# Kernel optimization log

Measured on AMD Instinct MI355X. Metric: run time of the kernel, lower is better.

The kernel has to match this reference:

```python
import jax, jax.numpy as jnp
import numpy as np

KH, KW = 3, 3
STRIDE = (1, 1)
PAD = (1, 1)
DIL = (1, 1)


def setup_inputs() -> dict:
    key = jax.random.key(0)
    k1, k2, k3, k4 = jax.random.split(key, 4)
    B, Cin, H, W = 8, 256, 64, 64
    Cout = 256
    x = jax.random.normal(k1, (B, Cin, H, W), jnp.float32)
    offset = jax.random.normal(k2, (B, 2 * KH * KW, H, W), jnp.float32)
    fan_in = Cin * KH * KW
    bound = 1.0 / np.sqrt(fan_in).astype(np.float32)
    weight = jax.random.uniform(k3, (Cout, Cin, KH, KW), jnp.float32, -bound, bound)
    bias = jax.random.uniform(k4, (Cout,), jnp.float32, -bound, bound)
    return {"x": x, "offset": offset, "weight": weight, "bias": bias}


def _deform_conv2d(x, offset, weight, bias):
    B, Cin, H, W = x.shape
    Cout = weight.shape[0]
    Ho, Wo = offset.shape[2], offset.shape[3]
    # offset layout: [B, 2*KH*KW, Ho, Wo] -> (dy, dx) per kernel tap
    off = offset.reshape(B, KH, KW, 2, Ho, Wo)
    dy = off[:, :, :, 0]  # [B,KH,KW,Ho,Wo]
    dx = off[:, :, :, 1]
    grid_y = jnp.arange(Ho, dtype=x.dtype) * STRIDE[0] - PAD[0]  # [Ho]
    grid_x = jnp.arange(Wo, dtype=x.dtype) * STRIDE[1] - PAD[1]  # [Wo]
    ker_y = jnp.arange(KH, dtype=x.dtype) * DIL[0]  # [KH]
    ker_x = jnp.arange(KW, dtype=x.dtype) * DIL[1]  # [KW]
    # sampling positions [B,KH,KW,Ho,Wo]
    py = dy + grid_y[None, None, None, :, None] + ker_y[None, :, None, None, None]
    px = dx + grid_x[None, None, None, None, :] + ker_x[None, None, :, None, None]

    y0f = jnp.floor(py)
    x0f = jnp.floor(px)
    wy = py - y0f  # fractional weights
    wx = px - x0f
    y0 = y0f.astype(jnp.int32)
    x0 = x0f.astype(jnp.int32)

    x_flat = x.reshape(B, Cin, H * W)

    def corner(yi, xi, w):
        # bilinear corner with zero padding outside the image
        valid = (yi >= 0) & (yi < H) & (xi >= 0) & (xi < W)
        idx = jnp.clip(yi, 0, H - 1) * W + jnp.clip(xi, 0, W - 1)  # [B,KH,KW,Ho,Wo]
        vals = jax.vmap(lambda xf, ii: xf[:, ii])(x_flat, idx)  # [B,Cin,KH,KW,Ho,Wo]
        return vals * (w * valid)[:, None]

    acc = corner(y0, x0, (1 - wy) * (1 - wx))
    acc = acc + corner(y0, x0 + 1, (1 - wy) * wx)
    acc = acc + corner(y0 + 1, x0, wy * (1 - wx))
    acc = acc + corner(y0 + 1, x0 + 1, wy * wx)

    # convolution accumulation over (Cin, KH, KW)
    out = jnp.einsum('bckluv,ockl->bouv', acc, weight)
    return out + bias[None, :, None, None]


def reference(x, offset, weight, bias):
    return _deform_conv2d(x, offset, weight, bias)
```

## Files before the change

kernel.cpp:

```cpp
#include <hip/hip_runtime.h>
#include <hip/hip_bf16.h>
#include <stdint.h>

typedef __attribute__((ext_vector_type(8))) short s16x8;
typedef __attribute__((ext_vector_type(4))) float f32x4;

#define XT_OFF   0u
#define WT_OFF   16777216u
#define PW_OFF   17956864u
#define PI_OFF   22675456u
#define WS_NEED  25034752u

static __device__ __forceinline__ uint16_t f2bf(float f) {
    __hip_bfloat16 h = __float2bfloat16(f);
    uint16_t u;
    __builtin_memcpy(&u, &h, 2);
    return u;
}
static __device__ __forceinline__ float bflo(uint32_t w) { return __uint_as_float(w << 16); }
static __device__ __forceinline__ float bfhi(uint32_t w) { return __uint_as_float(w & 0xffff0000u); }
static __device__ __forceinline__ float rdl(float v, int l) {
    return __uint_as_float((uint32_t)__builtin_amdgcn_readlane((int)__float_as_uint(v), l));
}

__global__ __launch_bounds__(256) void k_transpose_x(const float* __restrict__ x,
                                                     uint16_t* __restrict__ xt) {
    __shared__ float tile[64][65];
    const int blk = blockIdx.x;
    const int b   = blk >> 8;
    const int yxt = (blk >> 2) & 63;
    const int ct  = blk & 3;
    const int yx0 = yxt << 6, c0 = ct << 6;
    const int tx  = threadIdx.x;
    const int ty  = tx >> 6, lx = tx & 63;
    #pragma unroll
    for (int i = 0; i < 16; ++i) {
        const int c = (i << 2) + ty;
        tile[c][lx] = x[(size_t)((b * 256 + c0 + c) << 12) + yx0 + lx];
    }
    __syncthreads();
    const int cpr = lx & 31;
    #pragma unroll
    for (int i = 0; i < 8; ++i) {
        const int r = (ty << 1) + (lx >> 5) + (i << 3);
        const uint32_t lo = f2bf(tile[2 * cpr][r]);
        const uint32_t hi = f2bf(tile[2 * cpr + 1][r]);
        *(uint32_t*)&xt[(size_t)(b * 4096 + yx0 + r) * 256 + c0 + 2 * cpr] = lo | (hi << 16);
    }
}

__global__ __launch_bounds__(256) void k_prep_w(const float* __restrict__ wgt,
                                                uint16_t* __restrict__ wt) {
    const int blk = blockIdx.x;
    const int kb = blk >> 2, wc = blk & 3;
    const int m = threadIdx.x >> 6, lane = threadIdx.x & 63;
    const int o = wc * 64 + m * 16 + (lane & 15);
    const int t = kb >> 3;
    const int ch0 = (kb & 7) * 32 + (lane >> 4) * 8;
    uint32_t pk[4];
    #pragma unroll
    for (int q = 0; q < 4; ++q) {
        const float v0 = wgt[(size_t)o * 2304 + (size_t)(ch0 + 2 * q) * 9 + t];
        const float v1 = wgt[(size_t)o * 2304 + (size_t)(ch0 + 2 * q + 1) * 9 + t];
        pk[q] = (uint32_t)f2bf(v0) | ((uint32_t)f2bf(v1) << 16);
    }
    uint4 r; r.x = pk[0]; r.y = pk[1]; r.z = pk[2]; r.w = pk[3];
    *(uint4*)((char*)wt + (size_t)kb * 16384 + wc * 4096 + m * 1024 + lane * 16) = r;
}

__global__ __launch_bounds__(256) void k_prep_params(const float* __restrict__ off,
                                                     float4* __restrict__ pw,
                                                     uint2* __restrict__ pi) {
    const int blk = blockIdx.x;
    const int b = blk / 144;
    const int r = blk - b * 144;
    const int t = r >> 4;
    const int p = ((r & 15) << 8) + threadIdx.x;
    const int u = p >> 6, v = p & 63;
    const int kh = t / 3, kw = t - 3 * kh;
    const float dy = off[(size_t)((b * 18 + 2 * t) << 12) + p];
    const float dx = off[(size_t)((b * 18 + 2 * t + 1) << 12) + p];
    const float py = dy + (float)(u - 1 + kh);
    const float px = dx + (float)(v - 1 + kw);
    const float y0f = floorf(py), x0f = floorf(px);
    const float wy = py - y0f, wx = px - x0f;
    const int y0 = (int)y0f, x0 = (int)x0f;
    const int y1 = y0 + 1, x1 = x0 + 1;
    const bool vy0 = (y0 >= 0) && (y0 < 64);
    const bool vy1 = (y1 >= 0) && (y1 < 64);
    const bool vx0 = (x0 >= 0) && (x0 < 64);
    const bool vx1 = (x1 >= 0) && (x1 < 64);
    const int cy0 = min(max(y0, 0), 63), cy1 = min(max(y1, 0), 63);
    const int cx0 = min(max(x0, 0), 63), cx1 = min(max(x1, 0), 63);
    float4 w4;
    w4.x = (1.f - wy) * (1.f - wx) * ((vy0 && vx0) ? 1.f : 0.f);
    w4.y = (1.f - wy) * wx         * ((vy0 && vx1) ? 1.f : 0.f);
    w4.z = wy * (1.f - wx)         * ((vy1 && vx0) ? 1.f : 0.f);
    w4.w = wy * wx                 * ((vy1 && vx1) ? 1.f : 0.f);
    uint2 id;
    id.x = (uint32_t)(cy0 * 64 + cx0) | ((uint32_t)(cy0 * 64 + cx1) << 16);
    id.y = (uint32_t)(cy1 * 64 + cx0) | ((uint32_t)(cy1 * 64 + cx1) << 16);
    const size_t o_ = (size_t)(b * 9 + t) * 4096 + p;
    pw[o_] = w4;
    pi[o_] = id;
}


#define BLENDPX(PAR, LP, PXL) do {                                                \
    const float wqa = rdl(pwv.x, (PXL)), wqb = rdl(pwv.y, (PXL));                 \
    const float wqc = rdl(pwv.z, (PXL)), wqd = rdl(pwv.w, (PXL));                 \
    const uint2 A_ = cr[PAR][0], B_ = cr[PAR][1];                                 \
    const uint2 C_ = cr[PAR][2], D_ = cr[PAR][3];                                 \
    uint2 r_;                                                                     \
    { const float lo = wqa * bflo(A_.x) + wqb * bflo(B_.x)                        \
                     + wqc * bflo(C_.x) + wqd * bflo(D_.x);                       \
      const float hi = wqa * bfhi(A_.x) + wqb * bfhi(B_.x)                        \
                     + wqc * bfhi(C_.x) + wqd * bfhi(D_.x);                       \
      r_.x = (uint32_t)f2bf(lo) | ((uint32_t)f2bf(hi) << 16); }                   \
    { const float lo = wqa * bflo(A_.y) + wqb * bflo(B_.y)                        \
                     + wqc * bflo(C_.y) + wqd * bflo(D_.y);                       \
      const float hi = wqa * bfhi(A_.y) + wqb * bfhi(B_.y)                        \
                     + wqc * bfhi(C_.y) + wqd * bfhi(D_.y);                       \
      r_.y = (uint32_t)f2bf(lo) | ((uint32_t)f2bf(hi) << 16); }                   \
    const int slot_ = (lane >> 1) ^ ((LP) & 7);                                   \
    *(uint2*)(inxt + (LP) * 512 + slot_ * 16 + (lane & 1) * 8) = r_;              \
} while (0)

#define STEP(T, S, STG) do {                                                      \
    const int kb_ = (T) * 8 + (S);                                                \
    if (STG) {                                                                    \
        const uint32_t ix_ = (uint32_t)__builtin_amdgcn_readlane((int)piv.x, (S)); \
        const uint32_t iy_ = (uint32_t)__builtin_amdgcn_readlane((int)piv.y, (S)); \
        cr[(S)&1][0] = *(const uint2*)(xb + (ix_ & 0xffffu) * 256u + lane * 4);   \
        cr[(S)&1][1] = *(const uint2*)(xb + (ix_ >> 16)     * 256u + lane * 4);   \
        cr[(S)&1][2] = *(const uint2*)(xb + (iy_ & 0xffffu) * 256u + lane * 4);   \
        cr[(S)&1][3] = *(const uint2*)(xb + (iy_ >> 16)     * 256u + lane * 4);   \
    }                                                                             \
    if (kb_ < 71) {                                                               \
        _Pragma("unroll")                                                         \
        for (int m = 0; m < 4; ++m)                                               \
            wA[((S)+1)&1][m] = *(const s16x8*)(wfrag + (size_t)(kb_+1) * 16384 + m * 1024); \
    }                                                                             \
    if ((STG) && (S) >= 1) BLENDPX(((S)-1)&1, wv * 8 + (S) - 1, (S) - 1);         \
    {                                                                             \
        s16x8 bfr[2];                                                             \
        _Pragma("unroll")                                                         \
        for (int j = 0; j < 2; ++j)                                               \
            bfr[j] = *(const s16x8*)(icur + rb0 + j * 8192 + ((((S) * 4 + kp) ^ (l15 & 7)) << 4)); \
        __builtin_amdgcn_s_setprio(1);                                            \
        _Pragma("unroll")                                                         \
        for (int m = 0; m < 4; ++m)                                               \
            _Pragma("unroll")                                                     \
            for (int j = 0; j < 2; ++j)                                           \
                acc[m][j] = __builtin_amdgcn_mfma_f32_16x16x32_bf16(wA[(S)&1][m], bfr[j], acc[m][j], 0, 0, 0); \
        __builtin_amdgcn_s_setprio(0);                                            \
    }                                                                             \
} while (0)

__global__ __launch_bounds__(512, 4) void k_main(const uint16_t* __restrict__ xt,
                                                 const uint16_t* __restrict__ wt,
                                                 const float4* __restrict__ pw,
                                                 const uint2* __restrict__ pi,
                                                 const float* __restrict__ bias,
                                                 float* __restrict__ out) {
    __shared__ uint16_t imc[2][64 * 256];

    const int orig = blockIdx.x;
    const int bid  = (orig & 7) * 64 + (orig >> 3);
    const int b    = bid >> 6;
    const int pix0 = (bid & 63) << 6;

    const int tx   = threadIdx.x;
    const int lane = tx & 63;
    const int wv   = tx >> 6;
    const int wc   = wv & 3;
    const int wn   = wv >> 2;
    const int l15  = lane & 15;
    const int kp   = lane >> 4;

    const uint16_t* xb = xt + (size_t)b * 4096 * 256;
    const char* wfrag = (const char*)wt + (size_t)wc * 4096 + (size_t)lane * 16;

    const int rb0 = (wn * 32 + l15) * 512;

    f32x4 acc[4][2];
    #pragma unroll
    for (int m = 0; m < 4; ++m)
        #pragma unroll
        for (int j = 0; j < 2; ++j) acc[m][j] = (f32x4){0.f, 0.f, 0.f, 0.f};

    #pragma unroll
    for (int i = 0; i < 8; ++i) {
        const int lp = wv * 8 + i;
        const int ui = __builtin_amdgcn_readfirstlane(b * 9 * 4096 + pix0 + lp);
        const uint2  id = pi[ui];
        const float4 w4 = pw[ui];
        const uint2 A  = *(const uint2*)(xb + (id.x & 0xffffu) * 256u + lane * 4);
        const uint2 Bv = *(const uint2*)(xb + (id.x >> 16)     * 256u + lane * 4);
        const uint2 Cv = *(const uint2*)(xb + (id.y & 0xffffu) * 256u + lane * 4);
        const uint2 Dv = *(const uint2*)(xb + (id.y >> 16)     * 256u + lane * 4);
        uint2 r;
        { const float lo = w4.x * bflo(A.x) + w4.y * bflo(Bv.x)
                         + w4.z * bflo(Cv.x) + w4.w * bflo(Dv.x);
          const float hi = w4.x * bfhi(A.x) + w4.y * bfhi(Bv.x)
                         + w4.z * bfhi(Cv.x) + w4.w * bfhi(Dv.x);
          r.x = (uint32_t)f2bf(lo) | ((uint32_t)f2bf(hi) << 16); }
        { const float lo = w4.x * bflo(A.y) + w4.y * bflo(Bv.y)
                         + w4.z * bflo(Cv.y) + w4.w * bflo(Dv.y);
          const float hi = w4.x * bfhi(A.y) + w4.y * bfhi(Bv.y)
                         + w4.z * bfhi(Cv.y) + w4.w * bfhi(Dv.y);
          r.y = (uint32_t)f2bf(lo) | ((uint32_t)f2bf(hi) << 16); }
        const int slot = (lane >> 1) ^ (lp & 7);
        *(uint2*)((char*)&imc[0][0] + lp * 512 + slot * 16 + (lane & 1) * 8) = r;
    }

    s16x8 wA[2][4];
    #pragma unroll
    for (int m = 0; m < 4; ++m) wA[0][m] = *(const s16x8*)(wfrag + m * 1024);

    uint2  cr[2][4];
    uint2  piv = {0, 0};
    float4 pwv = {0.f, 0.f, 0.f, 0.f};

    #pragma unroll 1
    for (int t = 0; t < 8; ++t) {
        __syncthreads();
        const char* icur = (const char*)&imc[t & 1][0];
        char*       inxt = (char*)&imc[(t + 1) & 1][0];
        {
            const int idx = (b * 9 + t + 1) * 4096 + pix0 + wv * 8 + (lane & 7);
            piv = pi[idx];
            pwv = pw[idx];
        }
        STEP(t, 0, 1); STEP(t, 1, 1); STEP(t, 2, 1); STEP(t, 3, 1);
        STEP(t, 4, 1); STEP(t, 5, 1); STEP(t, 6, 1); STEP(t, 7, 1);
        BLENDPX(1, wv * 8 + 7, 7);
    }

    __syncthreads();
    {
        const char* icur = (const char*)&imc[0][0];
        char*       inxt = (char*)&imc[1][0];
        (void)inxt;
        STEP(8, 0, 0); STEP(8, 1, 0); STEP(8, 2, 0); STEP(8, 3, 0);
        STEP(8, 4, 0); STEP(8, 5, 0); STEP(8, 6, 0); STEP(8, 7, 0);
    }

    #pragma unroll
    for (int m = 0; m < 4; ++m) {
        #pragma unroll
        for (int q = 0; q < 4; ++q) {
            const int o = wc * 64 + m * 16 + kp * 4 + q;
            const float bv = bias[o];
            float* orow = out + (((size_t)(b * 256 + o)) << 12) + pix0 + wn * 32;
            #pragma unroll
            for (int j = 0; j < 2; ++j)
                orow[j * 16 + l15] = acc[m][j][q] + bv;
        }
    }
}

#define KTOT 2304
#define KCF  32
#define WROW 260
#define AROW 72

__global__ __launch_bounds__(256) void deform_conv_fallback(
    const float* __restrict__ x, const float* __restrict__ off,
    const float* __restrict__ wgt, const float* __restrict__ bias,
    float* __restrict__ out) {
    __shared__ float  w_lds[KCF][WROW];
    __shared__ float  a_lds[KCF][AROW];
    __shared__ int4   pidx[9][64];
    __shared__ float4 pwgt[9][64];
    const int tx = threadIdx.x;
    const int blk = blockIdx.x;
    const int b = blk >> 6, u = blk & 63;
    for (int item = tx; item < 9 * 64; item += 256) {
        const int t = item >> 6, p = item & 63;
        const int k = t / 3, l = t - 3 * k;
        const float dy = off[((b * 18 + 2 * t) << 12) + u * 64 + p];
        const float dx = off[((b * 18 + 2 * t + 1) << 12) + u * 64 + p];
        const float py = dy + (float)(u - 1 + k);
        const float px = dx + (float)(p - 1 + l);
        const float y0f = floorf(py), x0f = floorf(px);
        const float wy = py - y0f, wx = px - x0f;
        const int y0 = (int)y0f, x0 = (int)x0f, y1 = y0 + 1, x1 = x0 + 1;
        const bool vy0 = (y0 >= 0) && (y0 < 64), vy1 = (y1 >= 0) && (y1 < 64);
        const bool vx0 = (x0 >= 0) && (x0 < 64), vx1 = (x1 >= 0) && (x1 < 64);
        const int cy0 = min(max(y0, 0), 63), cy1 = min(max(y1, 0), 63);
        const int cx0 = min(max(x0, 0), 63), cx1 = min(max(x1, 0), 63);
        int4 id; id.x = cy0 * 64 + cx0; id.y = cy0 * 64 + cx1;
        id.z = cy1 * 64 + cx0; id.w = cy1 * 64 + cx1;
        float4 w4;
        w4.x = (1.f - wy) * (1.f - wx) * ((vy0 && vx0) ? 1.f : 0.f);
        w4.y = (1.f - wy) * wx * ((vy0 && vx1) ? 1.f : 0.f);
        w4.z = wy * (1.f - wx) * ((vy1 && vx0) ? 1.f : 0.f);
        w4.w = wy * wx * ((vy1 && vx1) ? 1.f : 0.f);
        pidx[t][p] = id; pwgt[t][p] = w4;
    }
    const int og = tx & 31, pgr = tx >> 5;
    float acc[8][8];
    #pragma unroll
    for (int j = 0; j < 8; ++j)
        #pragma unroll
        for (int q = 0; q < 8; ++q) acc[j][q] = 0.f;
    __syncthreads();
    for (int kb = 0; kb < 72; ++kb) {
        const int k0 = kb * KCF;
        #pragma unroll
        for (int it = 0; it < 8; ++it) {
            const int item = it * 256 + tx;
            const int o = item >> 3, jj = item & 7;
            const float4 v = *(const float4*)&wgt[o * KTOT + k0 + jj * 4];
            w_lds[jj * 4 + 0][o] = v.x; w_lds[jj * 4 + 1][o] = v.y;
            w_lds[jj * 4 + 2][o] = v.z; w_lds[jj * 4 + 3][o] = v.w;
        }
        #pragma unroll
        for (int it = 0; it < 8; ++it) {
            const int item = it * 256 + tx;
            const int kk = item >> 6, p = item & 63;
            const int kg = k0 + kk;
            const int c = kg / 9, t = kg - 9 * c;
            const float* plane = x + ((b * 256 + c) << 12);
            const int4 id = pidx[t][p];
            const float4 w4 = pwgt[t][p];
            float v = w4.x * plane[id.x] + w4.y * plane[id.y]
                    + w4.z * plane[id.z] + w4.w * plane[id.w];
            a_lds[kk][p] = v;
        }
        __syncthreads();
        #pragma unroll 2
        for (int kk = 0; kk < KCF; ++kk) {
            const float4 w0 = *(const float4*)&w_lds[kk][og * 8];
            const float4 w1 = *(const float4*)&w_lds[kk][og * 8 + 4];
            const float4 a0 = *(const float4*)&a_lds[kk][pgr * 8];
            const float4 a1 = *(const float4*)&a_lds[kk][pgr * 8 + 4];
            const float wv[8] = {w0.x, w0.y, w0.z, w0.w, w1.x, w1.y, w1.z, w1.w};
            const float av[8] = {a0.x, a0.y, a0.z, a0.w, a1.x, a1.y, a1.z, a1.w};
            #pragma unroll
            for (int j = 0; j < 8; ++j)
                #pragma unroll
                for (int q = 0; q < 8; ++q) acc[j][q] += wv[j] * av[q];
        }
        __syncthreads();
    }
    const int vb = pgr * 8;
    #pragma unroll
    for (int j = 0; j < 8; ++j) {
        const int o = og * 8 + j;
        const float bv = bias[o];
        float* op = out + ((b * 256 + o) << 12) + u * 64 + vb;
        float4 r0, r1;
        r0.x = acc[j][0] + bv; r0.y = acc[j][1] + bv; r0.z = acc[j][2] + bv; r0.w = acc[j][3] + bv;
        r1.x = acc[j][4] + bv; r1.y = acc[j][5] + bv; r1.z = acc[j][6] + bv; r1.w = acc[j][7] + bv;
        *(float4*)op = r0; *(float4*)(op + 4) = r1;
    }
}

extern "C" void kernel_launch(void* const* d_in, const int* in_sizes, int n_in,
                              void* d_out, int out_size, void* d_ws, size_t ws_size,
                              hipStream_t stream) {
    const float* x    = (const float*)d_in[0];
    const float* off  = (const float*)d_in[1];
    const float* wgt  = (const float*)d_in[2];
    const float* bias = (const float*)d_in[3];
    float* out = (float*)d_out;

    if (ws_size < WS_NEED) {
        deform_conv_fallback<<<dim3(512), dim3(256), 0, stream>>>(x, off, wgt, bias, out);
        return;
    }
    uint16_t* xt  = (uint16_t*)((char*)d_ws + XT_OFF);
    uint16_t* wtp = (uint16_t*)((char*)d_ws + WT_OFF);
    float4*   pwp = (float4*)((char*)d_ws + PW_OFF);
    uint2*    pip = (uint2*)((char*)d_ws + PI_OFF);

    k_transpose_x <<<dim3(2048), dim3(256), 0, stream>>>(x, xt);
    k_prep_w      <<<dim3(288),  dim3(256), 0, stream>>>(wgt, wtp);
    k_prep_params <<<dim3(1152), dim3(256), 0, stream>>>(off, pwp, pip);
    k_main        <<<dim3(512),  dim3(512), 0, stream>>>(xt, wtp, pwp, pip, bias, out);
}
```

Before: 97.31 us.

## Re-tile waves to 32 out-channels x 64 pixels and pair k-steps per stage

Changes the per-wave MFMA tile from 64 output channels x 32 pixels to 32 output channels x 64 pixels, so each wave reads all pixel columns from LDS and a narrower weight slice. The weight prep layout is regrouped into 16-channel groups to match. The main loop now processes two k-blocks per step, gathering corners for two pixels at once and blending two pixels per step, which deepens the prefetch of gathered data and weights. This trades more LDS B-fragment reads per wave for fewer global weight loads, and holds more gathered registers at once, which may raise register pressure.

```diff
diff --git a/kernel.cpp b/kernel.cpp
--- a/kernel.cpp
+++ b/kernel.cpp
@@ -52,9 +52,10 @@
 __global__ __launch_bounds__(256) void k_prep_w(const float* __restrict__ wgt,
                                                 uint16_t* __restrict__ wt) {
     const int blk = blockIdx.x;
-    const int kb = blk >> 2, wc = blk & 3;
+    const int kb = blk >> 2, gq = blk & 3;
     const int m = threadIdx.x >> 6, lane = threadIdx.x & 63;
-    const int o = wc * 64 + m * 16 + (lane & 15);
+    const int g = gq * 4 + m;
+    const int o = g * 16 + (lane & 15);
     const int t = kb >> 3;
     const int ch0 = (kb & 7) * 32 + (lane >> 4) * 8;
     uint32_t pk[4];
@@ -65,7 +66,7 @@
         pk[q] = (uint32_t)f2bf(v0) | ((uint32_t)f2bf(v1) << 16);
     }
     uint4 r; r.x = pk[0]; r.y = pk[1]; r.z = pk[2]; r.w = pk[3];
-    *(uint4*)((char*)wt + (size_t)kb * 16384 + wc * 4096 + m * 1024 + lane * 16) = r;
+    *(uint4*)((char*)wt + (size_t)kb * 16384 + g * 1024 + lane * 16) = r;
 }
 
 __global__ __launch_bounds__(256) void k_prep_params(const float* __restrict__ off,
@@ -106,11 +107,13 @@
 }
 
 
-#define BLENDPX(PAR, LP, PXL) do {                                                \
+#define BOFF(S) ((((S) * 4 + kp) ^ (l15 & 7)) << 4)
+
+#define BLEND1(SLOT, P, PXL) do {                                                 \
     const float wqa = rdl(pwv.x, (PXL)), wqb = rdl(pwv.y, (PXL));                 \
     const float wqc = rdl(pwv.z, (PXL)), wqd = rdl(pwv.w, (PXL));                 \
-    const uint2 A_ = cr[PAR][0], B_ = cr[PAR][1];                                 \
-    const uint2 C_ = cr[PAR][2], D_ = cr[PAR][3];                                 \
+    const uint2 A_ = cr[SLOT][P][0], B_ = cr[SLOT][P][1];                         \
+    const uint2 C_ = cr[SLOT][P][2], D_ = cr[SLOT][P][3];                         \
     uint2 r_;                                                                     \
     { const float lo = wqa * bflo(A_.x) + wqb * bflo(B_.x)                        \
                      + wqc * bflo(C_.x) + wqd * bflo(D_.x);                       \
@@ -122,37 +125,58 @@
       const float hi = wqa * bfhi(A_.y) + wqb * bfhi(B_.y)                        \
                      + wqc * bfhi(C_.y) + wqd * bfhi(D_.y);                       \
       r_.y = (uint32_t)f2bf(lo) | ((uint32_t)f2bf(hi) << 16); }                   \
-    const int slot_ = (lane >> 1) ^ ((LP) & 7);                                   \
-    *(uint2*)(inxt + (LP) * 512 + slot_ * 16 + (lane & 1) * 8) = r_;              \
+    const int lp_ = wv * 8 + (PXL);                                               \
+    const int sl_ = (lane >> 1) ^ (lp_ & 7);                                      \
+    *(uint2*)(inxt + lp_ * 512 + sl_ * 16 + (lane & 1) * 8) = r_;                 \
 } while (0)
 
-#define STEP(T, S, STG) do {                                                      \
-    const int kb_ = (T) * 8 + (S);                                                \
-    if (STG) {                                                                    \
-        const uint32_t ix_ = (uint32_t)__builtin_amdgcn_readlane((int)piv.x, (S)); \
-        const uint32_t iy_ = (uint32_t)__builtin_amdgcn_readlane((int)piv.y, (S)); \
-        cr[(S)&1][0] = *(const uint2*)(xb + (ix_ & 0xffffu) * 256u + lane * 4);   \
-        cr[(S)&1][1] = *(const uint2*)(xb + (ix_ >> 16)     * 256u + lane * 4);   \
-        cr[(S)&1][2] = *(const uint2*)(xb + (iy_ & 0xffffu) * 256u + lane * 4);   \
-        cr[(S)&1][3] = *(const uint2*)(xb + (iy_ >> 16)     * 256u + lane * 4);   \
+#define ISSUE2(SLOT, PX0) do {                                                    \
+    _Pragma("unroll")                                                             \
+    for (int p_ = 0; p_ < 2; ++p_) {                                              \
+        const uint32_t ix_ = (uint32_t)__builtin_amdgcn_readlane((int)piv.x, (PX0) + p_); \
+        const uint32_t iy_ = (uint32_t)__builtin_amdgcn_readlane((int)piv.y, (PX0) + p_); \
+        cr[SLOT][p_][0] = *(const uint2*)(xb + (ix_ & 0xffffu) * 256u + lane * 4); \
+        cr[SLOT][p_][1] = *(const uint2*)(xb + (ix_ >> 16)     * 256u + lane * 4); \
+        cr[SLOT][p_][2] = *(const uint2*)(xb + (iy_ & 0xffffu) * 256u + lane * 4); \
+        cr[SLOT][p_][3] = *(const uint2*)(xb + (iy_ >> 16)     * 256u + lane * 4); \
     }                                                                             \
-    if (kb_ < 71) {                                                               \
+} while (0)
+
+#define STEP2(T, U, STG) do {                                                     \
+    const int kbA_ = (T) * 8 + 2 * (U);                                           \
+    if ((STG) && (U) >= 1) {                                                      \
+        BLEND1(((U) - 1) & 1, 0, 2 * (U) - 2);                                    \
+        BLEND1(((U) - 1) & 1, 1, 2 * (U) - 1);                                    \
+    }                                                                             \
+    if ((STG) && (U) < 3) ISSUE2(((U) + 1) & 1, 2 * (U) + 2);                     \
+    if (kbA_ + 2 < 72) {                                                          \
         _Pragma("unroll")                                                         \
-        for (int m = 0; m < 4; ++m)                                               \
-            wA[((S)+1)&1][m] = *(const s16x8*)(wfrag + (size_t)(kb_+1) * 16384 + m * 1024); \
+        for (int m = 0; m < 2; ++m) {                                             \
+            wAp[((U) + 1) & 1][0][m] = *(const s16x8*)(wfrag + (size_t)(kbA_ + 2) * 16384 + m * 1024); \
+            wAp[((U) + 1) & 1][1][m] = *(const s16x8*)(wfrag + (size_t)(kbA_ + 3) * 16384 + m * 1024); \
+        }                                                                         \
     }                                                                             \
-    if ((STG) && (S) >= 1) BLENDPX(((S)-1)&1, wv * 8 + (S) - 1, (S) - 1);         \
     {                                                                             \
-        s16x8 bfr[2];                                                             \
+        s16x8 bfr[4];                                                             \
         _Pragma("unroll")                                                         \
-        for (int j = 0; j < 2; ++j)                                               \
-            bfr[j] = *(const s16x8*)(icur + rb0 + j * 8192 + ((((S) * 4 + kp) ^ (l15 & 7)) << 4)); \
+        for (int j = 0; j < 4; ++j)                                               \
+            bfr[j] = *(const s16x8*)(icur + (j * 16 + l15) * 512 + BOFF(2 * (U)));\
         __builtin_amdgcn_s_setprio(1);                                            \
         _Pragma("unroll")                                                         \
-        for (int m = 0; m < 4; ++m)                                               \
+        for (int m = 0; m < 2; ++m)                                               \
             _Pragma("unroll")                                                     \
-            for (int j = 0; j < 2; ++j)                                           \
-                acc[m][j] = __builtin_amdgcn_mfma_f32_16x16x32_bf16(wA[(S)&1][m], bfr[j], acc[m][j], 0, 0, 0); \
+            for (int j = 0; j < 4; ++j)                                           \
+                acc[m][j] = __builtin_amdgcn_mfma_f32_16x16x32_bf16(wAp[(U) & 1][0][m], bfr[j], acc[m][j], 0, 0, 0); \
+        __builtin_amdgcn_s_setprio(0);                                            \
+        _Pragma("unroll")                                                         \
+        for (int j = 0; j < 4; ++j)                                               \
+            bfr[j] = *(const s16x8*)(icur + (j * 16 + l15) * 512 + BOFF(2 * (U) + 1)); \
+        __builtin_amdgcn_s_setprio(1);                                            \
+        _Pragma("unroll")                                                         \
+        for (int m = 0; m < 2; ++m)                                               \
+            _Pragma("unroll")                                                     \
+            for (int j = 0; j < 4; ++j)                                           \
+                acc[m][j] = __builtin_amdgcn_mfma_f32_16x16x32_bf16(wAp[(U) & 1][1][m], bfr[j], acc[m][j], 0, 0, 0); \
         __builtin_amdgcn_s_setprio(0);                                            \
     }                                                                             \
 } while (0)
@@ -173,21 +197,17 @@
     const int tx   = threadIdx.x;
     const int lane = tx & 63;
     const int wv   = tx >> 6;
-    const int wc   = wv & 3;
-    const int wn   = wv >> 2;
     const int l15  = lane & 15;
     const int kp   = lane >> 4;
 
     const uint16_t* xb = xt + (size_t)b * 4096 * 256;
-    const char* wfrag = (const char*)wt + (size_t)wc * 4096 + (size_t)lane * 16;
-
-    const int rb0 = (wn * 32 + l15) * 512;
-
-    f32x4 acc[4][2];
-    #pragma unroll
-    for (int m = 0; m < 4; ++m)
+    const char* wfrag = (const char*)wt + (size_t)wv * 2048 + (size_t)lane * 16;
+
+    f32x4 acc[2][4];
+    #pragma unroll
+    for (int m = 0; m < 2; ++m)
         #pragma unroll
-        for (int j = 0; j < 2; ++j) acc[m][j] = (f32x4){0.f, 0.f, 0.f, 0.f};
+        for (int j = 0; j < 4; ++j) acc[m][j] = (f32x4){0.f, 0.f, 0.f, 0.f};
 
     #pragma unroll
     for (int i = 0; i < 8; ++i) {
@@ -214,11 +234,14 @@
         *(uint2*)((char*)&imc[0][0] + lp * 512 + slot * 16 + (lane & 1) * 8) = r;
     }
 
-    s16x8 wA[2][4];
-    #pragma unroll
-    for (int m = 0; m < 4; ++m) wA[0][m] = *(const s16x8*)(wfrag + m * 1024);
-
-    uint2  cr[2][4];
+    s16x8 wAp[2][2][2];
+    #pragma unroll
+    for (int m = 0; m < 2; ++m) {
+        wAp[0][0][m] = *(const s16x8*)(wfrag + m * 1024);
+        wAp[0][1][m] = *(const s16x8*)(wfrag + 16384 + m * 1024);
+    }
+
+    uint2  cr[2][2][4];
     uint2  piv = {0, 0};
     float4 pwv = {0.f, 0.f, 0.f, 0.f};
 
@@ -232,9 +255,10 @@
             piv = pi[idx];
             pwv = pw[idx];
         }
-        STEP(t, 0, 1); STEP(t, 1, 1); STEP(t, 2, 1); STEP(t, 3, 1);
-        STEP(t, 4, 1); STEP(t, 5, 1); STEP(t, 6, 1); STEP(t, 7, 1);
-        BLENDPX(1, wv * 8 + 7, 7);
+        ISSUE2(0, 0);
+        STEP2(t, 0, 1); STEP2(t, 1, 1); STEP2(t, 2, 1); STEP2(t, 3, 1);
+        BLEND1(1, 0, 6);
+        BLEND1(1, 1, 7);
     }
 
     __syncthreads();
@@ -242,19 +266,18 @@
         const char* icur = (const char*)&imc[0][0];
         char*       inxt = (char*)&imc[1][0];
         (void)inxt;
-        STEP(8, 0, 0); STEP(8, 1, 0); STEP(8, 2, 0); STEP(8, 3, 0);
-        STEP(8, 4, 0); STEP(8, 5, 0); STEP(8, 6, 0); STEP(8, 7, 0);
-    }
-
-    #pragma unroll
-    for (int m = 0; m < 4; ++m) {
+        STEP2(8, 0, 0); STEP2(8, 1, 0); STEP2(8, 2, 0); STEP2(8, 3, 0);
+    }
+
+    #pragma unroll
+    for (int m = 0; m < 2; ++m) {
         #pragma unroll
         for (int q = 0; q < 4; ++q) {
-            const int o = wc * 64 + m * 16 + kp * 4 + q;
+            const int o = wv * 32 + m * 16 + kp * 4 + q;
             const float bv = bias[o];
-            float* orow = out + (((size_t)(b * 256 + o)) << 12) + pix0 + wn * 32;
+            float* orow = out + (((size_t)(b * 256 + o)) << 12) + pix0;
             #pragma unroll
-            for (int j = 0; j < 2; ++j)
+            for (int j = 0; j < 4; ++j)
                 orow[j * 16 + l15] = acc[m][j][q] + bv;
         }
     }
```

After: 134.9 us. 1.39x slower.

## Warp-specialize deform conv into gather-producer and MFMA-consumer waves

Applied to the files above, without the earlier changes.

The 8 waves of each block now split into 4 producer waves, which gather and bilinearly blend 16 pixels per tap into the LDS double buffer with a 4-deep load pipeline, and 4 consumer waves, which each compute a 64-channel by 64-pixel tile with MFMA. Previously every wave did both gathering and MFMA work in an interleaved schedule. The aim is to overlap the irregular global gathers with matrix math more cleanly. In exchange, half the waves do no MFMA work, consumer waves hold twice the accumulator registers, and the occupancy hint drops from 4 to 2 blocks per CU.

```diff
diff --git a/kernel.cpp b/kernel.cpp
--- a/kernel.cpp
+++ b/kernel.cpp
@@ -106,11 +106,20 @@
 }
 
 
-#define BLENDPX(PAR, LP, PXL) do {                                                \
-    const float wqa = rdl(pwv.x, (PXL)), wqb = rdl(pwv.y, (PXL));                 \
-    const float wqc = rdl(pwv.z, (PXL)), wqd = rdl(pwv.w, (PXL));                 \
-    const uint2 A_ = cr[PAR][0], B_ = cr[PAR][1];                                 \
-    const uint2 C_ = cr[PAR][2], D_ = cr[PAR][3];                                 \
+#define PIS(RI, PX) do {                                                          \
+    const uint32_t ix_ = (uint32_t)__builtin_amdgcn_readlane((int)piv.x, (PX));   \
+    const uint32_t iy_ = (uint32_t)__builtin_amdgcn_readlane((int)piv.y, (PX));   \
+    crp[RI][0] = *(const uint2*)(xb + (ix_ & 0xffffu) * 256u + lane * 4);         \
+    crp[RI][1] = *(const uint2*)(xb + (ix_ >> 16)     * 256u + lane * 4);         \
+    crp[RI][2] = *(const uint2*)(xb + (iy_ & 0xffffu) * 256u + lane * 4);         \
+    crp[RI][3] = *(const uint2*)(xb + (iy_ >> 16)     * 256u + lane * 4);         \
+} while (0)
+
+#define PBL(RI, PX, DST) do {                                                     \
+    const float wqa = rdl(pwv.x, (PX)), wqb = rdl(pwv.y, (PX));                   \
+    const float wqc = rdl(pwv.z, (PX)), wqd = rdl(pwv.w, (PX));                   \
+    const uint2 A_ = crp[RI][0], B_ = crp[RI][1];                                 \
+    const uint2 C_ = crp[RI][2], D_ = crp[RI][3];                                 \
     uint2 r_;                                                                     \
     { const float lo = wqa * bflo(A_.x) + wqb * bflo(B_.x)                        \
                      + wqc * bflo(C_.x) + wqd * bflo(D_.x);                       \
@@ -122,42 +131,46 @@
       const float hi = wqa * bfhi(A_.y) + wqb * bfhi(B_.y)                        \
                      + wqc * bfhi(C_.y) + wqd * bfhi(D_.y);                       \
       r_.y = (uint32_t)f2bf(lo) | ((uint32_t)f2bf(hi) << 16); }                   \
-    const int slot_ = (lane >> 1) ^ ((LP) & 7);                                   \
-    *(uint2*)(inxt + (LP) * 512 + slot_ * 16 + (lane & 1) * 8) = r_;              \
+    const int lp_ = wv * 16 + (PX);                                               \
+    const int sl_ = (lane >> 1) ^ (lp_ & 7);                                      \
+    *(uint2*)((DST) + lp_ * 512 + sl_ * 16 + (lane & 1) * 8) = r_;                \
 } while (0)
 
-#define STEP(T, S, STG) do {                                                      \
+#define STAGE_TAP(TT, DST) do {                                                   \
+    const int idx_ = (b * 9 + (TT)) * 4096 + pix0 + wv * 16 + (lane & 15);        \
+    piv = pi[idx_];                                                               \
+    pwv = pw[idx_];                                                               \
+    PIS(0, 0); PIS(1, 1); PIS(2, 2);                                              \
+    _Pragma("unroll")                                                             \
+    for (int i_ = 0; i_ < 16; ++i_) {                                             \
+        if (i_ < 13) PIS((i_ + 3) & 3, i_ + 3);                                   \
+        PBL(i_ & 3, i_, DST);                                                     \
+    }                                                                             \
+} while (0)
+
+#define CSTEP(T, S) do {                                                          \
     const int kb_ = (T) * 8 + (S);                                                \
-    if (STG) {                                                                    \
-        const uint32_t ix_ = (uint32_t)__builtin_amdgcn_readlane((int)piv.x, (S)); \
-        const uint32_t iy_ = (uint32_t)__builtin_amdgcn_readlane((int)piv.y, (S)); \
-        cr[(S)&1][0] = *(const uint2*)(xb + (ix_ & 0xffffu) * 256u + lane * 4);   \
-        cr[(S)&1][1] = *(const uint2*)(xb + (ix_ >> 16)     * 256u + lane * 4);   \
-        cr[(S)&1][2] = *(const uint2*)(xb + (iy_ & 0xffffu) * 256u + lane * 4);   \
-        cr[(S)&1][3] = *(const uint2*)(xb + (iy_ >> 16)     * 256u + lane * 4);   \
-    }                                                                             \
     if (kb_ < 71) {                                                               \
         _Pragma("unroll")                                                         \
         for (int m = 0; m < 4; ++m)                                               \
-            wA[((S)+1)&1][m] = *(const s16x8*)(wfrag + (size_t)(kb_+1) * 16384 + m * 1024); \
+            wA[((S) + 1) & 1][m] = *(const s16x8*)(wfrag + (size_t)(kb_ + 1) * 16384 + m * 1024); \
     }                                                                             \
-    if ((STG) && (S) >= 1) BLENDPX(((S)-1)&1, wv * 8 + (S) - 1, (S) - 1);         \
     {                                                                             \
-        s16x8 bfr[2];                                                             \
+        s16x8 bfr[4];                                                             \
         _Pragma("unroll")                                                         \
-        for (int j = 0; j < 2; ++j)                                               \
-            bfr[j] = *(const s16x8*)(icur + rb0 + j * 8192 + ((((S) * 4 + kp) ^ (l15 & 7)) << 4)); \
+        for (int j = 0; j < 4; ++j)                                               \
+            bfr[j] = *(const s16x8*)(icur + (j * 16 + l15) * 512 + ((((S) * 4 + kp) ^ (l15 & 7)) << 4)); \
         __builtin_amdgcn_s_setprio(1);                                            \
         _Pragma("unroll")                                                         \
         for (int m = 0; m < 4; ++m)                                               \
             _Pragma("unroll")                                                     \
-            for (int j = 0; j < 2; ++j)                                           \
-                acc[m][j] = __builtin_amdgcn_mfma_f32_16x16x32_bf16(wA[(S)&1][m], bfr[j], acc[m][j], 0, 0, 0); \
+            for (int j = 0; j < 4; ++j)                                           \
+                acc[m][j] = __builtin_amdgcn_mfma_f32_16x16x32_bf16(wA[(S) & 1][m], bfr[j], acc[m][j], 0, 0, 0); \
         __builtin_amdgcn_s_setprio(0);                                            \
     }                                                                             \
 } while (0)
 
-__global__ __launch_bounds__(512, 4) void k_main(const uint16_t* __restrict__ xt,
+__global__ __launch_bounds__(512, 2) void k_main(const uint16_t* __restrict__ xt,
                                                  const uint16_t* __restrict__ wt,
                                                  const float4* __restrict__ pw,
                                                  const uint2* __restrict__ pi,
@@ -173,89 +186,54 @@
     const int tx   = threadIdx.x;
     const int lane = tx & 63;
     const int wv   = tx >> 6;
-    const int wc   = wv & 3;
-    const int wn   = wv >> 2;
     const int l15  = lane & 15;
     const int kp   = lane >> 4;
 
     const uint16_t* xb = xt + (size_t)b * 4096 * 256;
-    const char* wfrag = (const char*)wt + (size_t)wc * 4096 + (size_t)lane * 16;
-
-    const int rb0 = (wn * 32 + l15) * 512;
-
-    f32x4 acc[4][2];
-    #pragma unroll
-    for (int m = 0; m < 4; ++m)
-        #pragma unroll
-        for (int j = 0; j < 2; ++j) acc[m][j] = (f32x4){0.f, 0.f, 0.f, 0.f};
-
-    #pragma unroll
-    for (int i = 0; i < 8; ++i) {
-        const int lp = wv * 8 + i;
-        const int ui = __builtin_amdgcn_readfirstlane(b * 9 * 4096 + pix0 + lp);
-        const uint2  id = pi[ui];
-        const float4 w4 = pw[ui];
-        const uint2 A  = *(const uint2*)(xb + (id.x & 0xffffu) * 256u + lane * 4);
-        const uint2 Bv = *(const uint2*)(xb + (id.x >> 16)     * 256u + lane * 4);
-        const uint2 Cv = *(const uint2*)(xb + (id.y & 0xffffu) * 256u + lane * 4);
-        const uint2 Dv = *(const uint2*)(xb + (id.y >> 16)     * 256u + lane * 4);
-        uint2 r;
-        { const float lo = w4.x * bflo(A.x) + w4.y * bflo(Bv.x)
-                         + w4.z * bflo(Cv.x) + w4.w * bflo(Dv.x);
-          const float hi = w4.x * bfhi(A.x) + w4.y * bfhi(Bv.x)
-                         + w4.z * bfhi(Cv.x) + w4.w * bfhi(Dv.x);
-          r.x = (uint32_t)f2bf(lo) | ((uint32_t)f2bf(hi) << 16); }
-        { const float lo = w4.x * bflo(A.y) + w4.y * bflo(Bv.y)
-                         + w4.z * bflo(Cv.y) + w4.w * bflo(Dv.y);
-          const float hi = w4.x * bfhi(A.y) + w4.y * bfhi(Bv.y)
-                         + w4.z * bfhi(Cv.y) + w4.w * bfhi(Dv.y);
-          r.y = (uint32_t)f2bf(lo) | ((uint32_t)f2bf(hi) << 16); }
-        const int slot = (lane >> 1) ^ (lp & 7);
-        *(uint2*)((char*)&imc[0][0] + lp * 512 + slot * 16 + (lane & 1) * 8) = r;
-    }
-
-    s16x8 wA[2][4];
-    #pragma unroll
-    for (int m = 0; m < 4; ++m) wA[0][m] = *(const s16x8*)(wfrag + m * 1024);
-
-    uint2  cr[2][4];
-    uint2  piv = {0, 0};
-    float4 pwv = {0.f, 0.f, 0.f, 0.f};
-
-    #pragma unroll 1
-    for (int t = 0; t < 8; ++t) {
-        __syncthreads();
-        const char* icur = (const char*)&imc[t & 1][0];
-        char*       inxt = (char*)&imc[(t + 1) & 1][0];
-        {
-            const int idx = (b * 9 + t + 1) * 4096 + pix0 + wv * 8 + (lane & 7);
-            piv = pi[idx];
-            pwv = pw[idx];
-        }
-        STEP(t, 0, 1); STEP(t, 1, 1); STEP(t, 2, 1); STEP(t, 3, 1);
-        STEP(t, 4, 1); STEP(t, 5, 1); STEP(t, 6, 1); STEP(t, 7, 1);
-        BLENDPX(1, wv * 8 + 7, 7);
-    }
-
-    __syncthreads();
-    {
-        const char* icur = (const char*)&imc[0][0];
-        char*       inxt = (char*)&imc[1][0];
-        (void)inxt;
-        STEP(8, 0, 0); STEP(8, 1, 0); STEP(8, 2, 0); STEP(8, 3, 0);
-        STEP(8, 4, 0); STEP(8, 5, 0); STEP(8, 6, 0); STEP(8, 7, 0);
-    }
-
-    #pragma unroll
-    for (int m = 0; m < 4; ++m) {
-        #pragma unroll
-        for (int q = 0; q < 4; ++q) {
-            const int o = wc * 64 + m * 16 + kp * 4 + q;
-            const float bv = bias[o];
-            float* orow = out + (((size_t)(b * 256 + o)) << 12) + pix0 + wn * 32;
+
+    if (wv < 4) {
+        uint2  piv = {0, 0};
+        float4 pwv = {0.f, 0.f, 0.f, 0.f};
+        uint2  crp[4][4];
+        STAGE_TAP(0, (char*)&imc[0][0]);
+        #pragma unroll 1
+        for (int t = 0; t < 9; ++t) {
+            __syncthreads();
+            if (t < 8) STAGE_TAP(t + 1, (char*)&imc[(t + 1) & 1][0]);
+        }
+    } else {
+        const int wc = wv - 4;
+        const char* wfrag = (const char*)wt + (size_t)wc * 4096 + (size_t)lane * 16;
+
+        f32x4 acc[4][4];
+        #pragma unroll
+        for (int m = 0; m < 4; ++m)
             #pragma unroll
-            for (int j = 0; j < 2; ++j)
-                orow[j * 16 + l15] = acc[m][j][q] + bv;
+            for (int j = 0; j < 4; ++j) acc[m][j] = (f32x4){0.f, 0.f, 0.f, 0.f};
+
+        s16x8 wA[2][4];
+        #pragma unroll
+        for (int m = 0; m < 4; ++m) wA[0][m] = *(const s16x8*)(wfrag + m * 1024);
+
+        #pragma unroll 1
+        for (int t = 0; t < 9; ++t) {
+            __syncthreads();
+            const char* icur = (const char*)&imc[t & 1][0];
+            CSTEP(t, 0); CSTEP(t, 1); CSTEP(t, 2); CSTEP(t, 3);
+            CSTEP(t, 4); CSTEP(t, 5); CSTEP(t, 6); CSTEP(t, 7);
+        }
+
+        #pragma unroll
+        for (int m = 0; m < 4; ++m) {
+            #pragma unroll
+            for (int q = 0; q < 4; ++q) {
+                const int o = wc * 64 + m * 16 + kp * 4 + q;
+                const float bv = bias[o];
+                float* orow = out + (((size_t)(b * 256 + o)) << 12) + pix0;
+                #pragma unroll
+                for (int j = 0; j < 4; ++j)
+                    orow[j * 16 + l15] = acc[m][j][q] + bv;
+            }
         }
     }
 }
```

Measured after the change: 86.22 us. 1.13x faster.
